# Performance work log

Measured on AMD Instinct MI355X. Metric: run time of the kernel, lower is better.

## Reference

```python
import jax, jax.numpy as jnp
import numpy as np

N_NODES = 4096
DEG = 8                      # uniform CSR fanout
N_EDGES = N_NODES * DEG      # one hyperedge per sampled neighbor entry
FEAT = 64                    # base_model default input_dim
HID = 32
N_CLASSES = 2
N_SEEDS = 512


def setup_inputs() -> dict:
    key = jax.random.key(0)
    k_ind, k_x, k_w1, k_w2, k_seed = jax.random.split(key, 5)
    # valid CSR row pointers: uniform degree DEG, last entry == N_EDGES
    sub_indptr = (jnp.arange(N_NODES + 1, dtype=jnp.int32) * DEG)
    sub_indices = jax.random.randint(k_ind, (N_EDGES,), 0, N_NODES, dtype=jnp.int32)
    X = jax.random.normal(k_x, (N_NODES, FEAT), dtype=jnp.float32)
    W1 = jax.random.normal(k_w1, (FEAT, HID), dtype=jnp.float32) * 0.1
    b1 = jnp.zeros((HID,), jnp.float32)
    W2 = jax.random.normal(k_w2, (HID, N_CLASSES), dtype=jnp.float32) * 0.1
    b2 = jnp.zeros((N_CLASSES,), jnp.float32)
    seed_idx = jax.random.randint(k_seed, (N_SEEDS,), 0, N_NODES, dtype=jnp.int32)
    return {"sub_indptr": sub_indptr, "sub_indices": sub_indices, "X": X,
            "W1": W1, "b1": b1, "W2": W2, "b2": b2, "seed_idx": seed_idx}


def _build_incidence(sub_indptr, sub_indices, num_nodes, dtype):
    # Edge e is the e-th entry of sub_indices; its source node u is the CSR row
    # containing position e. Vectorizes the original nested Python loops.
    E = sub_indices.shape[0]
    e = jnp.arange(E)
    u = jnp.searchsorted(sub_indptr, e, side='right') - 1   # source node per edge
    v = sub_indices                                          # neighbor per edge
    inc = jnp.zeros((num_nodes, E), dtype)
    inc = inc.at[u, e].set(1.0).at[v, e].set(1.0)            # scalar scatter-writes, fused
    return inc


def reference(sub_indptr, sub_indices, X, W1, b1, W2, b2, seed_idx):
    num_nodes = X.shape[0]
    inc = _build_incidence(sub_indptr, sub_indices, num_nodes, X.dtype)  # [N, E]
    # 2-layer hypergraph conv (node -> hyperedge -> node message passing)
    h = jax.nn.relu(inc @ (inc.T @ (X @ W1)) + b1)           # [N, HID]
    full_logits = inc @ (inc.T @ (h @ W2)) + b2              # [N, C]
    # seed extraction: node_mapping lookup -> indexed gather
    return full_logits[seed_idx]                             # [B, C]
```

## Files before the change

### kernel.cpp

```cpp
#include <hip/hip_runtime.h>

#define N_NODES 4096
#define DEG 8
#define N_EDGES (N_NODES * DEG)
#define FEAT 64
#define HID 32
#define NC 2
#define N_SEEDS 512
#define BCAP 32


__global__ __launch_bounds__(256) void k1_gemm(const float* __restrict__ X,
                                               const float* __restrict__ W1,
                                               float* __restrict__ Z1,
                                               int* __restrict__ r) {
    __shared__ float W1s[FEAT * HID];
    int t = threadIdx.x;
    for (int i = t; i < FEAT * HID; i += 256) W1s[i] = W1[i];
    __syncthreads();
    int idx = blockIdx.x * 256 + t;
    int n = idx >> 5, h = idx & 31;
    const float4* x4 = (const float4*)(X + n * FEAT);
    float acc = 0.f;
#pragma unroll
    for (int q = 0; q < 16; ++q) {
        float4 xv = x4[q];
        acc += xv.x * W1s[(4 * q + 0) * HID + h];
        acc += xv.y * W1s[(4 * q + 1) * HID + h];
        acc += xv.z * W1s[(4 * q + 2) * HID + h];
        acc += xv.w * W1s[(4 * q + 3) * HID + h];
    }
    Z1[idx] = acc;
    if (idx < N_NODES) r[idx] = 0;
}

__global__ __launch_bounds__(256) void k2_build(const int* __restrict__ ind,
                                                int* __restrict__ r,
                                                unsigned short* __restrict__ bkt) {
    int e = blockIdx.x * 256 + threadIdx.x;
    int u = e >> 3;
    int v = ind[e];
    if (v != u) {
        int slot = atomicAdd(&r[v], 1);
        if (slot < BCAP) bkt[v * BCAP + slot] = (unsigned short)u;
    }
}

__global__ __launch_bounds__(256) void k3_hop1(const float* __restrict__ Z1,
                                               const int* __restrict__ ind,
                                               const int* __restrict__ r,
                                               const unsigned short* __restrict__ bkt,
                                               const float* __restrict__ pb1,
                                               const float* __restrict__ W2,
                                               float* __restrict__ Z2) {
    int idx = blockIdx.x * 256 + threadIdx.x;
    int n = idx >> 5, h = idx & 31;

    const int4* rp = (const int4*)(ind + n * DEG);
    int4 ra = rp[0], rb = rp[1];
    const uint4* bp = (const uint4*)(bkt + n * BCAP);
    uint4 w0 = bp[0], w1 = bp[1];
    int rn = r[n];
    float zn = Z1[idx];

    int vs[8] = {ra.x, ra.y, ra.z, ra.w, rb.x, rb.y, rb.z, rb.w};
    float zv[8];
#pragma unroll
    for (int d = 0; d < 8; ++d) zv[d] = Z1[vs[d] * HID + h];

    unsigned wd[8] = {w0.x, w0.y, w0.z, w0.w, w1.x, w1.y, w1.z, w1.w};
    float zi[16];
#pragma unroll
    for (int j = 0; j < 8; ++j) {
        zi[2 * j]     = Z1[(int)(wd[j] & 0xFFFu) * HID + h];
        zi[2 * j + 1] = Z1[(int)((wd[j] >> 16) & 0xFFFu) * HID + h];
    }

    float a = (float)(DEG + rn) * zn;
#pragma unroll
    for (int d = 0; d < 8; ++d) a += (vs[d] != n) ? zv[d] : 0.f;
    int rc = rn < BCAP ? rn : BCAP;
#pragma unroll
    for (int j = 0; j < 16; ++j) a += (j < rc) ? zi[j] : 0.f;

    if (rc > 16) {
        uint4 w2v = bp[2], w3v = bp[3];
        unsigned we[8] = {w2v.x, w2v.y, w2v.z, w2v.w, w3v.x, w3v.y, w3v.z, w3v.w};
#pragma unroll
        for (int j = 0; j < 8; ++j) {
            int b0 = 16 + 2 * j;
            float z0 = Z1[(int)(we[j] & 0xFFFu) * HID + h];
            float z1 = Z1[(int)((we[j] >> 16) & 0xFFFu) * HID + h];
            a += (b0     < rc) ? z0 : 0.f;
            a += (b0 + 1 < rc) ? z1 : 0.f;
        }
    }

    float hk = a + pb1[h];
    hk = hk > 0.f ? hk : 0.f;
    float t0 = hk * W2[h * NC + 0];
    float t1 = hk * W2[h * NC + 1];
#pragma unroll
    for (int off = 16; off > 0; off >>= 1) {
        t0 += __shfl_down(t0, off, 32);
        t1 += __shfl_down(t1, off, 32);
    }
    if (h == 0) *(float2*)(Z2 + n * NC) = make_float2(t0, t1);
}

__global__ __launch_bounds__(256) void k4_out(const float* __restrict__ Z2,
                                              const int* __restrict__ ind,
                                              const int* __restrict__ r,
                                              const unsigned short* __restrict__ bkt,
                                              const float* __restrict__ pb2,
                                              const int* __restrict__ seed,
                                              float* __restrict__ out) {
    int s = blockIdx.x * 256 + threadIdx.x;
    if (s >= N_SEEDS) return;
    int n = seed[s];

    const int4* rp = (const int4*)(ind + n * DEG);
    int4 ra = rp[0], rb = rp[1];
    const uint4* bp = (const uint4*)(bkt + n * BCAP);
    uint4 w0 = bp[0], w1 = bp[1];
    int rn = r[n];
    float2 z = *(const float2*)(Z2 + n * NC);

    int vs[8] = {ra.x, ra.y, ra.z, ra.w, rb.x, rb.y, rb.z, rb.w};
    float2 zv[8];
#pragma unroll
    for (int d = 0; d < 8; ++d) zv[d] = *(const float2*)(Z2 + vs[d] * NC);

    unsigned wd[8] = {w0.x, w0.y, w0.z, w0.w, w1.x, w1.y, w1.z, w1.w};
    float2 zi[16];
#pragma unroll
    for (int j = 0; j < 8; ++j) {
        zi[2 * j]     = *(const float2*)(Z2 + (int)(wd[j] & 0xFFFu) * NC);
        zi[2 * j + 1] = *(const float2*)(Z2 + (int)((wd[j] >> 16) & 0xFFFu) * NC);
    }

    float c0 = (float)(DEG + rn);
    float a0 = c0 * z.x, a1 = c0 * z.y;
#pragma unroll
    for (int d = 0; d < 8; ++d)
        if (vs[d] != n) { a0 += zv[d].x; a1 += zv[d].y; }
    int rc = rn < BCAP ? rn : BCAP;
#pragma unroll
    for (int j = 0; j < 16; ++j)
        if (j < rc) { a0 += zi[j].x; a1 += zi[j].y; }

    if (rc > 16) {
        uint4 w2v = bp[2], w3v = bp[3];
        unsigned we[8] = {w2v.x, w2v.y, w2v.z, w2v.w, w3v.x, w3v.y, w3v.z, w3v.w};
#pragma unroll
        for (int j = 0; j < 8; ++j) {
            int b0 = 16 + 2 * j;
            float2 z0 = *(const float2*)(Z2 + (int)(we[j] & 0xFFFu) * NC);
            float2 z1 = *(const float2*)(Z2 + (int)((we[j] >> 16) & 0xFFFu) * NC);
            if (b0     < rc) { a0 += z0.x; a1 += z0.y; }
            if (b0 + 1 < rc) { a0 += z1.x; a1 += z1.y; }
        }
    }

    out[s * NC + 0] = a0 + pb2[0];
    out[s * NC + 1] = a1 + pb2[1];
}

extern "C" void kernel_launch(void* const* d_in, const int* in_sizes, int n_in,
                              void* d_out, int out_size, void* d_ws, size_t ws_size,
                              hipStream_t stream) {
    const int*   ind  = (const int*)d_in[1];
    const float* X    = (const float*)d_in[2];
    const float* W1   = (const float*)d_in[3];
    const float* b1   = (const float*)d_in[4];
    const float* W2   = (const float*)d_in[5];
    const float* b2   = (const float*)d_in[6];
    const int*   seed = (const int*)d_in[7];
    float* out = (float*)d_out;

    char* ws = (char*)d_ws;
    float*          Z1  = (float*)(ws);
    float*          Z2  = (float*)(ws + 512 * 1024);
    int*            r   = (int*)(ws + 544 * 1024);
    unsigned short* bkt = (unsigned short*)(ws + 576 * 1024);

    k1_gemm <<<(N_NODES * HID) / 256, 256, 0, stream>>>(X, W1, Z1, r);
    k2_build<<<N_EDGES / 256,        256, 0, stream>>>(ind, r, bkt);
    k3_hop1 <<<(N_NODES * HID) / 256, 256, 0, stream>>>(Z1, ind, r, bkt, b1, W2, Z2);
    k4_out  <<<(N_SEEDS + 255) / 256, 256, 0, stream>>>(Z2, ind, r, bkt, b2, seed, out);
}
```

Baseline: 22.01 us.

## Fuse final hop into hop1 via seed-list scatter with atomics, drop k4

Removes the fourth kernel by having hop1 push each node's layer-2 contribution directly to the output rows of the seeds that are adjacent to it. A per-node seed list, tagged and built alongside the incidence buckets, makes this possible, and the output is pre-initialised with the bias in the first kernel. This saves one launch and the Z2 round trip. In exchange it adds float atomics on the output, an O(seeds) duplicate-count loop per seed, and a cap of 8 seeds per node, so order-dependent float summation and seed overflow are risks.

```diff
diff --git a/kernel.cpp b/kernel.cpp
--- a/kernel.cpp
+++ b/kernel.cpp
@@ -8,12 +8,17 @@
 #define NC 2
 #define N_SEEDS 512
 #define BCAP 32
+#define SCAP 8
+#define TAG 0x5A5A0000u
 
 
 __global__ __launch_bounds__(256) void k1_gemm(const float* __restrict__ X,
                                                const float* __restrict__ W1,
+                                               const float* __restrict__ pb2,
                                                float* __restrict__ Z1,
-                                               int* __restrict__ r) {
+                                               int* __restrict__ r,
+                                               unsigned int* __restrict__ seedlist,
+                                               float* __restrict__ out) {
     __shared__ float W1s[FEAT * HID];
     int t = threadIdx.x;
     for (int i = t; i < FEAT * HID; i += 256) W1s[i] = W1[i];
@@ -32,17 +37,57 @@
     }
     Z1[idx] = acc;
     if (idx < N_NODES) r[idx] = 0;
+    if (idx < N_NODES * SCAP) seedlist[idx] = 0u;
+    if (idx >= N_NODES && idx < N_NODES + N_SEEDS * NC) {
+        int o = idx - N_NODES;
+        out[o] = pb2[o & 1];
+    }
 }
 
 __global__ __launch_bounds__(256) void k2_build(const int* __restrict__ ind,
+                                                const int* __restrict__ seed,
                                                 int* __restrict__ r,
-                                                unsigned short* __restrict__ bkt) {
-    int e = blockIdx.x * 256 + threadIdx.x;
-    int u = e >> 3;
-    int v = ind[e];
-    if (v != u) {
-        int slot = atomicAdd(&r[v], 1);
-        if (slot < BCAP) bkt[v * BCAP + slot] = (unsigned short)u;
+                                                unsigned short* __restrict__ bkt,
+                                                unsigned int* __restrict__ seedlist) {
+    int b = blockIdx.x, t = threadIdx.x;
+    if (b < N_EDGES / 256) {
+        int e = b * 256 + t;
+        int u = e >> 3;
+        int v = ind[e];
+        if (v != u) {
+            int slot = atomicAdd(&r[v], 1);
+            if (slot < BCAP) bkt[v * BCAP + slot] = (unsigned short)u;
+        }
+    } else {
+        int s = (b - N_EDGES / 256) * 256 + t;
+        int n = seed[s];
+        int cnt = 0;
+#pragma unroll 8
+        for (int q = 0; q < N_SEEDS; q += 4) {
+            int4 sv = *(const int4*)(seed + q);
+            cnt += (q + 0 < s && sv.x == n);
+            cnt += (q + 1 < s && sv.y == n);
+            cnt += (q + 2 < s && sv.z == n);
+            cnt += (q + 3 < s && sv.w == n);
+        }
+        if (cnt < SCAP) seedlist[n * SCAP + cnt] = TAG | (unsigned)s;
+    }
+}
+
+__device__ __forceinline__ void scatter_one(const unsigned int* __restrict__ seedlist,
+                                            float* __restrict__ out,
+                                            int m, float coef, float t0, float t1) {
+    const uint4* sp = (const uint4*)(seedlist + m * SCAP);
+    uint4 s0 = sp[0], s1 = sp[1];
+    unsigned ww[8] = {s0.x, s0.y, s0.z, s0.w, s1.x, s1.y, s1.z, s1.w};
+#pragma unroll
+    for (int k = 0; k < 8; ++k) {
+        unsigned w = ww[k];
+        if ((w & 0xFFFF0000u) == TAG) {
+            int s = (int)(w & 0xFFFFu);
+            atomicAdd(&out[s * NC + 0], coef * t0);
+            atomicAdd(&out[s * NC + 1], coef * t1);
+        }
     }
 }
 
@@ -52,7 +97,8 @@
                                                const unsigned short* __restrict__ bkt,
                                                const float* __restrict__ pb1,
                                                const float* __restrict__ W2,
-                                               float* __restrict__ Z2) {
+                                               const unsigned int* __restrict__ seedlist,
+                                               float* __restrict__ out) {
     int idx = blockIdx.x * 256 + threadIdx.x;
     int n = idx >> 5, h = idx & 31;
 
@@ -102,68 +148,22 @@
     float t1 = hk * W2[h * NC + 1];
 #pragma unroll
     for (int off = 16; off > 0; off >>= 1) {
-        t0 += __shfl_down(t0, off, 32);
-        t1 += __shfl_down(t1, off, 32);
-    }
-    if (h == 0) *(float2*)(Z2 + n * NC) = make_float2(t0, t1);
-}
-
-__global__ __launch_bounds__(256) void k4_out(const float* __restrict__ Z2,
-                                              const int* __restrict__ ind,
-                                              const int* __restrict__ r,
-                                              const unsigned short* __restrict__ bkt,
-                                              const float* __restrict__ pb2,
-                                              const int* __restrict__ seed,
-                                              float* __restrict__ out) {
-    int s = blockIdx.x * 256 + threadIdx.x;
-    if (s >= N_SEEDS) return;
-    int n = seed[s];
-
-    const int4* rp = (const int4*)(ind + n * DEG);
-    int4 ra = rp[0], rb = rp[1];
-    const uint4* bp = (const uint4*)(bkt + n * BCAP);
-    uint4 w0 = bp[0], w1 = bp[1];
-    int rn = r[n];
-    float2 z = *(const float2*)(Z2 + n * NC);
-
-    int vs[8] = {ra.x, ra.y, ra.z, ra.w, rb.x, rb.y, rb.z, rb.w};
-    float2 zv[8];
-#pragma unroll
-    for (int d = 0; d < 8; ++d) zv[d] = *(const float2*)(Z2 + vs[d] * NC);
-
-    unsigned wd[8] = {w0.x, w0.y, w0.z, w0.w, w1.x, w1.y, w1.z, w1.w};
-    float2 zi[16];
-#pragma unroll
-    for (int j = 0; j < 8; ++j) {
-        zi[2 * j]     = *(const float2*)(Z2 + (int)(wd[j] & 0xFFFu) * NC);
-        zi[2 * j + 1] = *(const float2*)(Z2 + (int)((wd[j] >> 16) & 0xFFFu) * NC);
+        t0 += __shfl_xor(t0, off, 32);
+        t1 += __shfl_xor(t1, off, 32);
     }
 
-    float c0 = (float)(DEG + rn);
-    float a0 = c0 * z.x, a1 = c0 * z.y;
-#pragma unroll
-    for (int d = 0; d < 8; ++d)
-        if (vs[d] != n) { a0 += zv[d].x; a1 += zv[d].y; }
-    int rc = rn < BCAP ? rn : BCAP;
-#pragma unroll
-    for (int j = 0; j < 16; ++j)
-        if (j < rc) { a0 += zi[j].x; a1 += zi[j].y; }
-
-    if (rc > 16) {
-        uint4 w2v = bp[2], w3v = bp[3];
-        unsigned we[8] = {w2v.x, w2v.y, w2v.z, w2v.w, w3v.x, w3v.y, w3v.z, w3v.w};
-#pragma unroll
-        for (int j = 0; j < 8; ++j) {
-            int b0 = 16 + 2 * j;
-            float2 z0 = *(const float2*)(Z2 + (int)(we[j] & 0xFFFu) * NC);
-            float2 z1 = *(const float2*)(Z2 + (int)((we[j] >> 16) & 0xFFFu) * NC);
-            if (b0     < rc) { a0 += z0.x; a1 += z0.y; }
-            if (b0 + 1 < rc) { a0 += z1.x; a1 += z1.y; }
-        }
+    {
+        int m; float coef; bool valid;
+        if (h == 0)      { m = n;                      coef = (float)(DEG + rn); valid = true; }
+        else if (h <= 8) { m = ind[n * DEG + (h - 1)]; coef = 1.f;               valid = (m != n); }
+        else             { int j = h - 9; valid = (j < rc);
+                           m = valid ? (int)bkt[n * BCAP + j] : 0; coef = 1.f; }
+        if (valid) scatter_one(seedlist, out, m, coef, t0, t1);
     }
-
-    out[s * NC + 0] = a0 + pb2[0];
-    out[s * NC + 1] = a1 + pb2[1];
+    if (h <= 8) {
+        int j = 23 + h;
+        if (j < rc) scatter_one(seedlist, out, (int)bkt[n * BCAP + j], 1.f, t0, t1);
+    }
 }
 
 extern "C" void kernel_launch(void* const* d_in, const int* in_sizes, int n_in,
@@ -180,12 +180,11 @@
 
     char* ws = (char*)d_ws;
     float*          Z1  = (float*)(ws);
-    float*          Z2  = (float*)(ws + 512 * 1024);
-    int*            r   = (int*)(ws + 544 * 1024);
-    unsigned short* bkt = (unsigned short*)(ws + 576 * 1024);
+    int*            r   = (int*)(ws + 512 * 1024);
+    unsigned short* bkt = (unsigned short*)(ws + 528 * 1024);
+    unsigned int*   sl  = (unsigned int*)(ws + 784 * 1024);
 
-    k1_gemm <<<(N_NODES * HID) / 256, 256, 0, stream>>>(X, W1, Z1, r);
-    k2_build<<<N_EDGES / 256,        256, 0, stream>>>(ind, r, bkt);
-    k3_hop1 <<<(N_NODES * HID) / 256, 256, 0, stream>>>(Z1, ind, r, bkt, b1, W2, Z2);
-    k4_out  <<<(N_SEEDS + 255) / 256, 256, 0, stream>>>(Z2, ind, r, bkt, b2, seed, out);
+    k1_gemm <<<(N_NODES * HID) / 256, 256, 0, stream>>>(X, W1, b2, Z1, r, sl, out);
+    k2_build<<<N_EDGES / 256 + 2,     256, 0, stream>>>(ind, seed, r, bkt, sl);
+    k3_hop1 <<<(N_NODES * HID) / 256, 256, 0, stream>>>(Z1, ind, r, bkt, b1, W2, sl, out);
 }
```

Result: slower. 33.36 us (+51.6%).

## Fuse GEMM with bucket build and compute layer two only for seed neighborhoods

Applied to the files above, without the earlier changes.

The first launch runs the X@W1 GEMM and the reverse-adjacency bucket build in one grid. Build blocks each own 32 nodes, scan all edges, and collect incidence in shared memory instead of using global atomics. The second launch computes hop-1 hidden features only for each seed's neighborhood, one block per seed, and combines them into the output. This drops the full-graph hop-1 pass and cuts four launches to two. The cost is that each build block reads all of ind, and nodes shared by several seeds are recomputed.

```diff
diff --git a/kernel.cpp b/kernel.cpp
--- a/kernel.cpp
+++ b/kernel.cpp
@@ -9,161 +9,152 @@
 #define N_SEEDS 512
 #define BCAP 32
 
+#define GEMM_BLOCKS 512
+#define BUILD_BLOCKS 128
+#define OWN 32
 
-__global__ __launch_bounds__(256) void k1_gemm(const float* __restrict__ X,
-                                               const float* __restrict__ W1,
-                                               float* __restrict__ Z1,
-                                               int* __restrict__ r) {
-    __shared__ float W1s[FEAT * HID];
+
+__global__ __launch_bounds__(256) void d1_gemm_build(
+        const float* __restrict__ X, const float* __restrict__ W1,
+        const int* __restrict__ ind,
+        float* __restrict__ Z1, int* __restrict__ r,
+        unsigned short* __restrict__ bkt) {
     int t = threadIdx.x;
-    for (int i = t; i < FEAT * HID; i += 256) W1s[i] = W1[i];
-    __syncthreads();
-    int idx = blockIdx.x * 256 + t;
-    int n = idx >> 5, h = idx & 31;
-    const float4* x4 = (const float4*)(X + n * FEAT);
-    float acc = 0.f;
+    if (blockIdx.x < GEMM_BLOCKS) {
+        __shared__ float W1s[FEAT * HID];
+        for (int i = t; i < FEAT * HID; i += 256) W1s[i] = W1[i];
+        __syncthreads();
+        int idx = blockIdx.x * 256 + t;
+        int n = idx >> 5, h = idx & 31;
+        const float4* x4 = (const float4*)(X + n * FEAT);
+        float acc = 0.f;
 #pragma unroll
-    for (int q = 0; q < 16; ++q) {
-        float4 xv = x4[q];
-        acc += xv.x * W1s[(4 * q + 0) * HID + h];
-        acc += xv.y * W1s[(4 * q + 1) * HID + h];
-        acc += xv.z * W1s[(4 * q + 2) * HID + h];
-        acc += xv.w * W1s[(4 * q + 3) * HID + h];
-    }
-    Z1[idx] = acc;
-    if (idx < N_NODES) r[idx] = 0;
-}
-
-__global__ __launch_bounds__(256) void k2_build(const int* __restrict__ ind,
-                                                int* __restrict__ r,
-                                                unsigned short* __restrict__ bkt) {
-    int e = blockIdx.x * 256 + threadIdx.x;
-    int u = e >> 3;
-    int v = ind[e];
-    if (v != u) {
-        int slot = atomicAdd(&r[v], 1);
-        if (slot < BCAP) bkt[v * BCAP + slot] = (unsigned short)u;
+        for (int q = 0; q < 16; ++q) {
+            float4 xv = x4[q];
+            acc += xv.x * W1s[(4 * q + 0) * HID + h];
+            acc += xv.y * W1s[(4 * q + 1) * HID + h];
+            acc += xv.z * W1s[(4 * q + 2) * HID + h];
+            acc += xv.w * W1s[(4 * q + 3) * HID + h];
+        }
+        Z1[idx] = acc;
+    } else {
+        __shared__ __align__(16) unsigned short lb[OWN * BCAP];
+        __shared__ int lc[OWN];
+        int b = blockIdx.x - GEMM_BLOCKS;
+        int lo = b * OWN;
+        if (t < OWN) lc[t] = 0;
+        __syncthreads();
+#pragma unroll 4
+        for (int i = 0; i < N_EDGES / 256; ++i) {
+            int e = i * 256 + t;
+            int v = ind[e];
+            unsigned dv = (unsigned)(v - lo);
+            int u = e >> 3;
+            if (dv < OWN && v != u) {
+                int slot = atomicAdd(&lc[dv], 1);
+                if (slot < BCAP) lb[dv * BCAP + slot] = (unsigned short)u;
+            }
+        }
+        __syncthreads();
+        if (t < OWN) r[lo + t] = lc[t];
+        ((uint2*)(bkt + lo * BCAP))[t] = ((const uint2*)lb)[t];
     }
 }
 
-__global__ __launch_bounds__(256) void k3_hop1(const float* __restrict__ Z1,
-                                               const int* __restrict__ ind,
-                                               const int* __restrict__ r,
-                                               const unsigned short* __restrict__ bkt,
-                                               const float* __restrict__ pb1,
-                                               const float* __restrict__ W2,
-                                               float* __restrict__ Z2) {
-    int idx = blockIdx.x * 256 + threadIdx.x;
-    int n = idx >> 5, h = idx & 31;
+__global__ __launch_bounds__(256) void d2_seed(
+        const float* __restrict__ Z1, const int* __restrict__ ind,
+        const int* __restrict__ r, const unsigned short* __restrict__ bkt,
+        const float* __restrict__ pb1, const float* __restrict__ W2,
+        const float* __restrict__ pb2, const int* __restrict__ seed,
+        float* __restrict__ out) {
+    int s = blockIdx.x;
+    int t = threadIdx.x;
+    int g = t >> 5, h = t & 31;
 
-    const int4* rp = (const int4*)(ind + n * DEG);
-    int4 ra = rp[0], rb = rp[1];
-    const uint4* bp = (const uint4*)(bkt + n * BCAP);
-    uint4 w0 = bp[0], w1 = bp[1];
+    __shared__ int   cm[9 + BCAP];
+    __shared__ float cc[9 + BCAP];
+    __shared__ float accs[8][2];
+
+    int n = seed[s];
     int rn = r[n];
-    float zn = Z1[idx];
+    int rcn = rn < BCAP ? rn : BCAP;
+    int nc = 9 + rcn;
+    if (t == 0) { cm[0] = n; cc[0] = (float)(DEG + rn); }
+    if (t >= 1 && t < 9) {
+        int v = ind[n * DEG + t - 1];
+        cm[t] = v; cc[t] = (v != n) ? 1.f : 0.f;
+    }
+    if (t >= 9 && t < nc) { cm[t] = (int)bkt[n * BCAP + (t - 9)]; cc[t] = 1.f; }
+    __syncthreads();
 
-    int vs[8] = {ra.x, ra.y, ra.z, ra.w, rb.x, rb.y, rb.z, rb.w};
-    float zv[8];
+    float s0 = 0.f, s1 = 0.f;
+    for (int base = 0; base < nc; base += 8) {
+        int ci = base + g;
+        if (ci < nc && cc[ci] != 0.f) {
+            int m = cm[ci];
+            float coef = cc[ci];
+            const int4* rp = (const int4*)(ind + m * DEG);
+            int4 ra = rp[0], rb = rp[1];
+            const uint4* bp = (const uint4*)(bkt + m * BCAP);
+            uint4 w0 = bp[0], w1 = bp[1];
+            int rm = r[m];
+            float zm = Z1[m * HID + h];
+
+            int vs[8] = {ra.x, ra.y, ra.z, ra.w, rb.x, rb.y, rb.z, rb.w};
+            float zv[8];
 #pragma unroll
-    for (int d = 0; d < 8; ++d) zv[d] = Z1[vs[d] * HID + h];
+            for (int d = 0; d < 8; ++d) zv[d] = Z1[vs[d] * HID + h];
 
-    unsigned wd[8] = {w0.x, w0.y, w0.z, w0.w, w1.x, w1.y, w1.z, w1.w};
-    float zi[16];
+            unsigned wd[8] = {w0.x, w0.y, w0.z, w0.w, w1.x, w1.y, w1.z, w1.w};
+            float zi[16];
 #pragma unroll
-    for (int j = 0; j < 8; ++j) {
-        zi[2 * j]     = Z1[(int)(wd[j] & 0xFFFu) * HID + h];
-        zi[2 * j + 1] = Z1[(int)((wd[j] >> 16) & 0xFFFu) * HID + h];
-    }
+            for (int j = 0; j < 8; ++j) {
+                zi[2 * j]     = Z1[(int)(wd[j] & 0xFFFu) * HID + h];
+                zi[2 * j + 1] = Z1[(int)((wd[j] >> 16) & 0xFFFu) * HID + h];
+            }
 
-    float a = (float)(DEG + rn) * zn;
+            float a = (float)(DEG + rm) * zm;
 #pragma unroll
-    for (int d = 0; d < 8; ++d) a += (vs[d] != n) ? zv[d] : 0.f;
-    int rc = rn < BCAP ? rn : BCAP;
+            for (int d = 0; d < 8; ++d) a += (vs[d] != m) ? zv[d] : 0.f;
+            int rc = rm < BCAP ? rm : BCAP;
 #pragma unroll
-    for (int j = 0; j < 16; ++j) a += (j < rc) ? zi[j] : 0.f;
+            for (int j = 0; j < 16; ++j) a += (j < rc) ? zi[j] : 0.f;
 
-    if (rc > 16) {
-        uint4 w2v = bp[2], w3v = bp[3];
-        unsigned we[8] = {w2v.x, w2v.y, w2v.z, w2v.w, w3v.x, w3v.y, w3v.z, w3v.w};
+            if (rc > 16) {
+                uint4 w2v = bp[2], w3v = bp[3];
+                unsigned we[8] = {w2v.x, w2v.y, w2v.z, w2v.w,
+                                  w3v.x, w3v.y, w3v.z, w3v.w};
 #pragma unroll
-        for (int j = 0; j < 8; ++j) {
-            int b0 = 16 + 2 * j;
-            float z0 = Z1[(int)(we[j] & 0xFFFu) * HID + h];
-            float z1 = Z1[(int)((we[j] >> 16) & 0xFFFu) * HID + h];
-            a += (b0     < rc) ? z0 : 0.f;
-            a += (b0 + 1 < rc) ? z1 : 0.f;
+                for (int j = 0; j < 8; ++j) {
+                    int b0 = 16 + 2 * j;
+                    float z0 = Z1[(int)(we[j] & 0xFFFu) * HID + h];
+                    float z1 = Z1[(int)((we[j] >> 16) & 0xFFFu) * HID + h];
+                    a += (b0     < rc) ? z0 : 0.f;
+                    a += (b0 + 1 < rc) ? z1 : 0.f;
+                }
+            }
+
+            float hk = a + pb1[h];
+            hk = hk > 0.f ? hk : 0.f;
+            float t0 = hk * W2[h * NC + 0];
+            float t1 = hk * W2[h * NC + 1];
+#pragma unroll
+            for (int off = 16; off > 0; off >>= 1) {
+                t0 += __shfl_down(t0, off, 32);
+                t1 += __shfl_down(t1, off, 32);
+            }
+            if (h == 0) { s0 += coef * t0; s1 += coef * t1; }
         }
     }
-
-    float hk = a + pb1[h];
-    hk = hk > 0.f ? hk : 0.f;
-    float t0 = hk * W2[h * NC + 0];
-    float t1 = hk * W2[h * NC + 1];
+    if (h == 0) { accs[g][0] = s0; accs[g][1] = s1; }
+    __syncthreads();
+    if (t == 0) {
+        float o0 = pb2[0], o1 = pb2[1];
 #pragma unroll
-    for (int off = 16; off > 0; off >>= 1) {
-        t0 += __shfl_down(t0, off, 32);
-        t1 += __shfl_down(t1, off, 32);
+        for (int gg = 0; gg < 8; ++gg) { o0 += accs[gg][0]; o1 += accs[gg][1]; }
+        out[s * NC + 0] = o0;
+        out[s * NC + 1] = o1;
     }
-    if (h == 0) *(float2*)(Z2 + n * NC) = make_float2(t0, t1);
-}
-
-__global__ __launch_bounds__(256) void k4_out(const float* __restrict__ Z2,
-                                              const int* __restrict__ ind,
-                                              const int* __restrict__ r,
-                                              const unsigned short* __restrict__ bkt,
-                                              const float* __restrict__ pb2,
-                                              const int* __restrict__ seed,
-                                              float* __restrict__ out) {
-    int s = blockIdx.x * 256 + threadIdx.x;
-    if (s >= N_SEEDS) return;
-    int n = seed[s];
-
-    const int4* rp = (const int4*)(ind + n * DEG);
-    int4 ra = rp[0], rb = rp[1];
-    const uint4* bp = (const uint4*)(bkt + n * BCAP);
-    uint4 w0 = bp[0], w1 = bp[1];
-    int rn = r[n];
-    float2 z = *(const float2*)(Z2 + n * NC);
-
-    int vs[8] = {ra.x, ra.y, ra.z, ra.w, rb.x, rb.y, rb.z, rb.w};
-    float2 zv[8];
-#pragma unroll
-    for (int d = 0; d < 8; ++d) zv[d] = *(const float2*)(Z2 + vs[d] * NC);
-
-    unsigned wd[8] = {w0.x, w0.y, w0.z, w0.w, w1.x, w1.y, w1.z, w1.w};
-    float2 zi[16];
-#pragma unroll
-    for (int j = 0; j < 8; ++j) {
-        zi[2 * j]     = *(const float2*)(Z2 + (int)(wd[j] & 0xFFFu) * NC);
-        zi[2 * j + 1] = *(const float2*)(Z2 + (int)((wd[j] >> 16) & 0xFFFu) * NC);
-    }
-
-    float c0 = (float)(DEG + rn);
-    float a0 = c0 * z.x, a1 = c0 * z.y;
-#pragma unroll
-    for (int d = 0; d < 8; ++d)
-        if (vs[d] != n) { a0 += zv[d].x; a1 += zv[d].y; }
-    int rc = rn < BCAP ? rn : BCAP;
-#pragma unroll
-    for (int j = 0; j < 16; ++j)
-        if (j < rc) { a0 += zi[j].x; a1 += zi[j].y; }
-
-    if (rc > 16) {
-        uint4 w2v = bp[2], w3v = bp[3];
-        unsigned we[8] = {w2v.x, w2v.y, w2v.z, w2v.w, w3v.x, w3v.y, w3v.z, w3v.w};
-#pragma unroll
-        for (int j = 0; j < 8; ++j) {
-            int b0 = 16 + 2 * j;
-            float2 z0 = *(const float2*)(Z2 + (int)(we[j] & 0xFFFu) * NC);
-            float2 z1 = *(const float2*)(Z2 + (int)((we[j] >> 16) & 0xFFFu) * NC);
-            if (b0     < rc) { a0 += z0.x; a1 += z0.y; }
-            if (b0 + 1 < rc) { a0 += z1.x; a1 += z1.y; }
-        }
-    }
-
-    out[s * NC + 0] = a0 + pb2[0];
-    out[s * NC + 1] = a1 + pb2[1];
 }
 
 extern "C" void kernel_launch(void* const* d_in, const int* in_sizes, int n_in,
@@ -180,12 +171,9 @@
 
     char* ws = (char*)d_ws;
     float*          Z1  = (float*)(ws);
-    float*          Z2  = (float*)(ws + 512 * 1024);
-    int*            r   = (int*)(ws + 544 * 1024);
-    unsigned short* bkt = (unsigned short*)(ws + 576 * 1024);
+    int*            r   = (int*)(ws + 512 * 1024);
+    unsigned short* bkt = (unsigned short*)(ws + 544 * 1024);
 
-    k1_gemm <<<(N_NODES * HID) / 256, 256, 0, stream>>>(X, W1, Z1, r);
-    k2_build<<<N_EDGES / 256,        256, 0, stream>>>(ind, r, bkt);
-    k3_hop1 <<<(N_NODES * HID) / 256, 256, 0, stream>>>(Z1, ind, r, bkt, b1, W2, Z2);
-    k4_out  <<<(N_SEEDS + 255) / 256, 256, 0, stream>>>(Z2, ind, r, bkt, b2, seed, out);
+    d1_gemm_build<<<GEMM_BLOCKS + BUILD_BLOCKS, 256, 0, stream>>>(X, W1, ind, Z1, r, bkt);
+    d2_seed      <<<N_SEEDS,                    256, 0, stream>>>(Z1, ind, r, bkt, b1, W2, b2, seed, out);
 }
```

Result: slower. 32.93 us (+49.6%).

## Fuse GEMM and bucket build into one launch with LDS-owned node buckets

Applied to the files above, without the earlier changes.

Merges the X@W1 GEMM and the reverse-adjacency bucket build into a single kernel whose blocks split by role: 512 GEMM blocks and 128 build blocks. Each build block owns 32 destination nodes, scans the whole index array, and accumulates counts and buckets with shared-memory atomics, then writes them out coalesced. This drops one kernel launch and the global-memory atomics and zero-init dependency. In exchange each build block rereads the full 128KB index array, and bucket order now differs between runs.

```diff
diff --git a/kernel.cpp b/kernel.cpp
--- a/kernel.cpp
+++ b/kernel.cpp
@@ -9,40 +9,61 @@
 #define N_SEEDS 512
 #define BCAP 32
 
-
-__global__ __launch_bounds__(256) void k1_gemm(const float* __restrict__ X,
-                                               const float* __restrict__ W1,
-                                               float* __restrict__ Z1,
-                                               int* __restrict__ r) {
-    __shared__ float W1s[FEAT * HID];
+#define GEMM_BLOCKS 512
+#define BUILD_BLOCKS 128
+#define OWN 32
+
+
+__global__ __launch_bounds__(256) void d1_gemm_build(
+        const float* __restrict__ X, const float* __restrict__ W1,
+        const int* __restrict__ ind,
+        float* __restrict__ Z1, int* __restrict__ r,
+        unsigned short* __restrict__ bkt) {
     int t = threadIdx.x;
-    for (int i = t; i < FEAT * HID; i += 256) W1s[i] = W1[i];
-    __syncthreads();
-    int idx = blockIdx.x * 256 + t;
-    int n = idx >> 5, h = idx & 31;
-    const float4* x4 = (const float4*)(X + n * FEAT);
-    float acc = 0.f;
-#pragma unroll
-    for (int q = 0; q < 16; ++q) {
-        float4 xv = x4[q];
-        acc += xv.x * W1s[(4 * q + 0) * HID + h];
-        acc += xv.y * W1s[(4 * q + 1) * HID + h];
-        acc += xv.z * W1s[(4 * q + 2) * HID + h];
-        acc += xv.w * W1s[(4 * q + 3) * HID + h];
-    }
-    Z1[idx] = acc;
-    if (idx < N_NODES) r[idx] = 0;
-}
-
-__global__ __launch_bounds__(256) void k2_build(const int* __restrict__ ind,
-                                                int* __restrict__ r,
-                                                unsigned short* __restrict__ bkt) {
-    int e = blockIdx.x * 256 + threadIdx.x;
-    int u = e >> 3;
-    int v = ind[e];
-    if (v != u) {
-        int slot = atomicAdd(&r[v], 1);
-        if (slot < BCAP) bkt[v * BCAP + slot] = (unsigned short)u;
+    if (blockIdx.x < GEMM_BLOCKS) {
+        __shared__ float W1s[FEAT * HID];
+        for (int i = t; i < FEAT * HID; i += 256) W1s[i] = W1[i];
+        __syncthreads();
+        int idx = blockIdx.x * 256 + t;
+        int n = idx >> 5, h = idx & 31;
+        const float4* x4 = (const float4*)(X + n * FEAT);
+        float acc = 0.f;
+#pragma unroll
+        for (int q = 0; q < 16; ++q) {
+            float4 xv = x4[q];
+            acc += xv.x * W1s[(4 * q + 0) * HID + h];
+            acc += xv.y * W1s[(4 * q + 1) * HID + h];
+            acc += xv.z * W1s[(4 * q + 2) * HID + h];
+            acc += xv.w * W1s[(4 * q + 3) * HID + h];
+        }
+        Z1[idx] = acc;
+    } else {
+        __shared__ __align__(16) unsigned short lb[OWN * BCAP];
+        __shared__ int lc[OWN];
+        int b = blockIdx.x - GEMM_BLOCKS;
+        int lo = b * OWN;
+        if (t < OWN) lc[t] = 0;
+        __syncthreads();
+        const int4* ind4 = (const int4*)ind;
+#pragma unroll 8
+        for (int i = 0; i < N_EDGES / 4 / 256; ++i) {
+            int4 q = ind4[i * 256 + t];
+            int e0 = (i * 256 + t) * 4;
+            int vv[4] = {q.x, q.y, q.z, q.w};
+#pragma unroll
+            for (int j = 0; j < 4; ++j) {
+                int v = vv[j];
+                unsigned dv = (unsigned)(v - lo);
+                int u = (e0 + j) >> 3;
+                if (dv < OWN && v != u) {
+                    int slot = atomicAdd(&lc[dv], 1);
+                    if (slot < BCAP) lb[dv * BCAP + slot] = (unsigned short)u;
+                }
+            }
+        }
+        __syncthreads();
+        if (t < OWN) r[lo + t] = lc[t];
+        ((uint2*)(bkt + lo * BCAP))[t] = ((const uint2*)lb)[t];
     }
 }
 
@@ -184,8 +205,7 @@
     int*            r   = (int*)(ws + 544 * 1024);
     unsigned short* bkt = (unsigned short*)(ws + 576 * 1024);
 
-    k1_gemm <<<(N_NODES * HID) / 256, 256, 0, stream>>>(X, W1, Z1, r);
-    k2_build<<<N_EDGES / 256,        256, 0, stream>>>(ind, r, bkt);
-    k3_hop1 <<<(N_NODES * HID) / 256, 256, 0, stream>>>(Z1, ind, r, bkt, b1, W2, Z2);
-    k4_out  <<<(N_SEEDS + 255) / 256, 256, 0, stream>>>(Z2, ind, r, bkt, b2, seed, out);
-}
+    d1_gemm_build<<<GEMM_BLOCKS + BUILD_BLOCKS, 256, 0, stream>>>(X, W1, ind, Z1, r, bkt);
+    k3_hop1      <<<(N_NODES * HID) / 256,      256, 0, stream>>>(Z1, ind, r, bkt, b1, W2, Z2);
+    k4_out       <<<(N_SEEDS + 255) / 256,      256, 0, stream>>>(Z2, ind, r, bkt, b2, seed, out);
+}
```

Result: slower. 25.87 us (+17.6%).
